# Kernel tuning notes

Hardware: AMD Instinct MI355X
Metric: run time of the kernel (lower is better)

## Reference

```python
import jax, jax.numpy as jnp
import numpy as np

N = 2048   # number of proposals
D = 128    # appearance feature dim
DK = 64    # key/query dim
DG = 64    # geometric embedding dim
SD = 8     # single relation output dim = appear_dim / N_r = 128/16


def setup_inputs() -> dict:
    key = jax.random.key(0)
    ks = jax.random.split(key, 10)
    s = jnp.float32(0.05)
    return {
        "appearance_feature": jax.random.normal(ks[0], (N, D), jnp.float32),
        "geometric_feature": jax.random.uniform(ks[1], (N, N, DG), jnp.float32),
        "Wv": jax.random.normal(ks[2], (D, SD), jnp.float32) * s,
        "bv": jnp.zeros((SD,), jnp.float32),
        "Wk": jax.random.normal(ks[3], (D, DK), jnp.float32) * s,
        "bk": jnp.zeros((DK,), jnp.float32),
        "Wq": jax.random.normal(ks[4], (D, DK), jnp.float32) * s,
        "bq": jnp.zeros((DK,), jnp.float32),
        "Wg": jax.random.normal(ks[5], (DG, 1), jnp.float32) * s,
        "bg": jnp.zeros((1,), jnp.float32),
    }


def reference(appearance_feature, geometric_feature, Wv, bv, Wk, bk, Wq, bq, Wg, bg):
    n = geometric_feature.shape[0]
    # value projection: [N, SD]
    appear = appearance_feature @ Wv + bv
    # key/query projections: [N, DK]
    k = appearance_feature @ Wk + bk
    q = appearance_feature @ Wq + bq
    # appearance attention logits: [N, N]
    w_A = (k @ q.T) * (1.0 / jnp.sqrt(jnp.float32(DK)))
    # geometric gate: relu(W_G(geom)) -> [N, N]
    w_G = jax.nn.relu(
        (geometric_feature.reshape(-1, DG) @ Wg + bg).reshape(n, n)
    )
    # gated exp, normalized over axis 0 (as in the source: torch.sum(w_nominator, 0))
    w_nom = w_G * jnp.exp(w_A)
    w = w_nom / jnp.sum(w_nom, axis=0, keepdims=True)
    # weighted sum of values: [N, SD]
    return w @ appear
```

## Files before the change

### kernel.cpp

```cpp
#include <hip/hip_runtime.h>

#define N 2048
#define D 128
#define DK 64
#define DG 64
#define SD 8
#define TI 8
#define TJ 256

typedef float f4v __attribute__((ext_vector_type(4)));

__global__ __launch_bounds__(128) void proj_kernel(
    const float* __restrict__ A,
    const float* __restrict__ Wv, const float* __restrict__ bv,
    const float* __restrict__ Wk, const float* __restrict__ bk,
    const float* __restrict__ Wq, const float* __restrict__ bq,
    float* __restrict__ kout, float* __restrict__ qout, float* __restrict__ vout)
{
    __shared__ float arow[D];
    const int i = blockIdx.x;
    const int t = threadIdx.x;
    arow[t] = A[(size_t)i * D + t];
    __syncthreads();
    for (int e = t; e < 2 * DK + SD; e += 128) {
        const float* W; const float* b; int od; int col;
        if (e < DK)            { W = Wk; b = bk; od = DK; col = e; }
        else if (e < 2 * DK)   { W = Wq; b = bq; od = DK; col = e - DK; }
        else                   { W = Wv; b = bv; od = SD; col = e - 2 * DK; }
        float acc = 0.f;
        #pragma unroll 8
        for (int c = 0; c < D; ++c) acc += arow[c] * W[c * od + col];
        acc += b[col];
        if (e < DK)          kout[(size_t)i * DK + col] = acc;
        else if (e < 2 * DK) qout[(size_t)i * DK + col] = acc;
        else                 vout[(size_t)i * SD + col] = acc;
    }
}

__global__ __launch_bounds__(256) void gate_kernel(
    const float* __restrict__ geom,
    const float* __restrict__ Wg, const float* __restrict__ bg,
    const float* __restrict__ kin, const float* __restrict__ qin,
    float* __restrict__ w_nom, float* __restrict__ colpartial)
{
    __shared__ float wA[TI * TJ];
    __shared__ float kt[TI * DK];
    const int tid = threadIdx.x;
    const int j0 = blockIdx.x * TJ;
    const int i0 = blockIdx.y * TI;

    for (int e = tid; e < TI * DK; e += 256) kt[e] = kin[(size_t)i0 * DK + e];
    __syncthreads();

    {
        float acc[TI];
        #pragma unroll
        for (int r = 0; r < TI; ++r) acc[r] = 0.f;
        const f4v* ktv = (const f4v*)kt;
        const f4v* qrow = (const f4v*)(qin + (size_t)(j0 + tid) * DK);
        f4v qv[16];
        #pragma unroll
        for (int m = 0; m < 16; ++m) qv[m] = qrow[m];
        #pragma unroll
        for (int r = 0; r < TI; ++r) {
            float p = 0.f;
            #pragma unroll
            for (int m = 0; m < 16; ++m) {
                f4v kv = ktv[r * 16 + m];
                p += kv.x * qv[m].x + kv.y * qv[m].y + kv.z * qv[m].z + kv.w * qv[m].w;
            }
            acc[r] = p;
        }
        #pragma unroll
        for (int r = 0; r < TI; ++r) wA[r * TJ + tid] = expf(acc[r] * 0.125f);
    }
    __syncthreads();

    const int group = tid >> 4;
    const int sub = tid & 15;
    const f4v wg4 = ((const f4v*)Wg)[sub];
    const float bgv = bg[0];

    float colacc[16];
    #pragma unroll
    for (int cc = 0; cc < 16; ++cc) colacc[cc] = 0.f;

    for (int ii = 0; ii < TI; ++ii) {
        const f4v* grow = (const f4v*)(geom + ((size_t)(i0 + ii) * N + j0) * DG);
        f4v g[16];
        #pragma unroll
        for (int cc = 0; cc < 16; ++cc)
            g[cc] = __builtin_nontemporal_load(grow + (size_t)(cc * 16 + group) * 16 + sub);
        #pragma unroll
        for (int cc = 0; cc < 16; ++cc) {
            float s = g[cc].x * wg4.x + g[cc].y * wg4.y + g[cc].z * wg4.z + g[cc].w * wg4.w;
            s += __shfl_xor(s, 1);
            s += __shfl_xor(s, 2);
            s += __shfl_xor(s, 4);
            s += __shfl_xor(s, 8);
            s += bgv;
            s = fmaxf(s, 0.f);
            const int jl = cc * 16 + group;
            const float val = s * wA[ii * TJ + jl];
            colacc[cc] += val;
            if (sub == 0) wA[ii * TJ + jl] = val;
        }
    }
    if (sub == 0) {
        #pragma unroll
        for (int cc = 0; cc < 16; ++cc)
            colpartial[(size_t)blockIdx.y * N + j0 + cc * 16 + group] = colacc[cc];
    }
    __syncthreads();
    {
        const f4v* src = (const f4v*)wA;
        #pragma unroll
        for (int r = 0; r < TI * TJ / 4; r += 256) {
            const int idx = r + tid;
            const int row = idx >> 6;
            const int col = idx & 63;
            ((f4v*)(w_nom + (size_t)(i0 + row) * N + j0))[col] = src[idx];
        }
    }
}

__global__ __launch_bounds__(256) void colsum_kernel(
    const float* __restrict__ colpartial, float* __restrict__ colrcp)
{
    const int j = blockIdx.x * 256 + threadIdx.x;
    float acc = 0.f;
    #pragma unroll 8
    for (int r = 0; r < N / TI; ++r) acc += colpartial[(size_t)r * N + j];
    colrcp[j] = 1.0f / acc;
}

__global__ __launch_bounds__(256) void out_kernel(
    const float* __restrict__ w_nom, const float* __restrict__ colrcp,
    const float* __restrict__ appear, float* __restrict__ out)
{
    const int i = blockIdx.x;
    const int t = threadIdx.x;
    float acc[SD];
    #pragma unroll
    for (int s = 0; s < SD; ++s) acc[s] = 0.f;

    #pragma unroll
    for (int jj = 0; jj < N / (256 * 4); ++jj) {
        const int j4 = jj * 256 + t;
        const f4v wn = ((const f4v*)(w_nom + (size_t)i * N))[j4];
        const f4v rc = ((const f4v*)colrcp)[j4];
        const float w0 = wn.x * rc.x, w1 = wn.y * rc.y, w2 = wn.z * rc.z, w3 = wn.w * rc.w;
        const int j = j4 * 4;
        const f4v* a0 = (const f4v*)(appear + (size_t)j * SD);
        f4v r0 = a0[0], r1 = a0[1];
        f4v r2 = a0[2], r3 = a0[3];
        f4v r4 = a0[4], r5 = a0[5];
        f4v r6 = a0[6], r7 = a0[7];
        acc[0] += w0 * r0.x + w1 * r2.x + w2 * r4.x + w3 * r6.x;
        acc[1] += w0 * r0.y + w1 * r2.y + w2 * r4.y + w3 * r6.y;
        acc[2] += w0 * r0.z + w1 * r2.z + w2 * r4.z + w3 * r6.z;
        acc[3] += w0 * r0.w + w1 * r2.w + w2 * r4.w + w3 * r6.w;
        acc[4] += w0 * r1.x + w1 * r3.x + w2 * r5.x + w3 * r7.x;
        acc[5] += w0 * r1.y + w1 * r3.y + w2 * r5.y + w3 * r7.y;
        acc[6] += w0 * r1.z + w1 * r3.z + w2 * r5.z + w3 * r7.z;
        acc[7] += w0 * r1.w + w1 * r3.w + w2 * r5.w + w3 * r7.w;
    }
    #pragma unroll
    for (int s = 0; s < SD; ++s) {
        #pragma unroll
        for (int off = 32; off >= 1; off >>= 1)
            acc[s] += __shfl_down(acc[s], off);
    }
    __shared__ float red[4][SD];
    const int wave = t >> 6;
    const int lane = t & 63;
    if (lane == 0) {
        #pragma unroll
        for (int s = 0; s < SD; ++s) red[wave][s] = acc[s];
    }
    __syncthreads();
    if (t < SD) out[(size_t)i * SD + t] = red[0][t] + red[1][t] + red[2][t] + red[3][t];
}

extern "C" void kernel_launch(void* const* d_in, const int* in_sizes, int n_in,
                              void* d_out, int out_size, void* d_ws, size_t ws_size,
                              hipStream_t stream) {
    const float* A    = (const float*)d_in[0];
    const float* geom = (const float*)d_in[1];
    const float* Wv   = (const float*)d_in[2];
    const float* bv   = (const float*)d_in[3];
    const float* Wk   = (const float*)d_in[4];
    const float* bk   = (const float*)d_in[5];
    const float* Wq   = (const float*)d_in[6];
    const float* bq   = (const float*)d_in[7];
    const float* Wg   = (const float*)d_in[8];
    const float* bg   = (const float*)d_in[9];
    float* out = (float*)d_out;

    float* ws = (float*)d_ws;
    float* kbuf       = ws;
    float* qbuf       = kbuf + (size_t)N * DK;
    float* appear     = qbuf + (size_t)N * DK;
    float* w_nom      = appear + (size_t)N * SD;
    float* colpartial = w_nom + (size_t)N * N;
    float* colrcp     = colpartial + (size_t)(N / TI) * N;

    proj_kernel<<<N, 128, 0, stream>>>(A, Wv, bv, Wk, bk, Wq, bq, kbuf, qbuf, appear);
    gate_kernel<<<dim3(N / TJ, N / TI), 256, 0, stream>>>(geom, Wg, bg, kbuf, qbuf,
                                                          w_nom, colpartial);
    colsum_kernel<<<N / 256, 256, 0, stream>>>(colpartial, colrcp);
    out_kernel<<<N, 256, 0, stream>>>(w_nom, colrcp, appear, out);
}
```

Baseline: 243.7 us.

## Double-buffer geometric loads and prefetch before QK compute in gate kernel

```diff
diff --git a/kernel.cpp b/kernel.cpp
--- a/kernel.cpp
+++ b/kernel.cpp
@@ -49,18 +49,52 @@
     const int j0 = blockIdx.x * TJ;
     const int i0 = blockIdx.y * TI;
 
+    const int wv  = tid >> 6;
+    const int grp = (tid >> 4) & 3;
+    const int sub = tid & 15;
+
+    const f4v* qrow = (const f4v*)(qin + (size_t)(j0 + tid) * DK);
+    f4v qv[16];
+    #pragma unroll
+    for (int m = 0; m < 16; ++m) qv[m] = qrow[m];
+
+    f4v gb0[8], gb1[8];
+
+#define G_ISSUE(buf, step) do {                                                   \
+        const int ii_ = (step) >> 1, h_ = (step) & 1;                             \
+        const f4v* grow_ = (const f4v*)(geom + ((size_t)(i0 + ii_) * N + j0) * DG);\
+        _Pragma("unroll")                                                         \
+        for (int c_ = 0; c_ < 8; ++c_) {                                          \
+            const int jl_ = wv * 64 + (h_ * 8 + c_) * 4 + grp;                    \
+            buf[c_] = grow_[(size_t)jl_ * 16 + sub];                              \
+        } } while (0)
+
+#define G_CONSUME(buf, step) do {                                                 \
+        const int ii_ = (step) >> 1, h_ = (step) & 1;                             \
+        _Pragma("unroll")                                                         \
+        for (int c_ = 0; c_ < 8; ++c_) {                                          \
+            const int cc_ = h_ * 8 + c_;                                          \
+            const int jl_ = wv * 64 + cc_ * 4 + grp;                              \
+            float s_ = buf[c_].x * wg4.x + buf[c_].y * wg4.y +                    \
+                       buf[c_].z * wg4.z + buf[c_].w * wg4.w;                     \
+            s_ += __shfl_xor(s_, 1);                                              \
+            s_ += __shfl_xor(s_, 2);                                              \
+            s_ += __shfl_xor(s_, 4);                                              \
+            s_ += __shfl_xor(s_, 8);                                              \
+            s_ = fmaxf(s_ + bgv, 0.f);                                            \
+            const float val_ = s_ * wA[ii_ * TJ + jl_];                           \
+            colacc[cc_] += val_;                                                  \
+            if (sub == 0) wA[ii_ * TJ + jl_] = val_;                              \
+        } } while (0)
+
+    G_ISSUE(gb0, 0);
+
     for (int e = tid; e < TI * DK; e += 256) kt[e] = kin[(size_t)i0 * DK + e];
     __syncthreads();
 
     {
+        const f4v* ktv = (const f4v*)kt;
         float acc[TI];
-        #pragma unroll
-        for (int r = 0; r < TI; ++r) acc[r] = 0.f;
-        const f4v* ktv = (const f4v*)kt;
-        const f4v* qrow = (const f4v*)(qin + (size_t)(j0 + tid) * DK);
-        f4v qv[16];
-        #pragma unroll
-        for (int m = 0; m < 16; ++m) qv[m] = qrow[m];
         #pragma unroll
         for (int r = 0; r < TI; ++r) {
             float p = 0.f;
@@ -76,8 +110,6 @@
     }
     __syncthreads();
 
-    const int group = tid >> 4;
-    const int sub = tid & 15;
     const f4v wg4 = ((const f4v*)Wg)[sub];
     const float bgv = bg[0];
 
@@ -85,33 +117,26 @@
     #pragma unroll
     for (int cc = 0; cc < 16; ++cc) colacc[cc] = 0.f;
 
-    for (int ii = 0; ii < TI; ++ii) {
-        const f4v* grow = (const f4v*)(geom + ((size_t)(i0 + ii) * N + j0) * DG);
-        f4v g[16];
+    #pragma unroll
+    for (int step = 0; step < 2 * TI; ++step) {
+        if ((step & 1) == 0) {
+            if (step + 1 < 2 * TI) G_ISSUE(gb1, step + 1);
+            G_CONSUME(gb0, step);
+        } else {
+            if (step + 1 < 2 * TI) G_ISSUE(gb0, step + 1);
+            G_CONSUME(gb1, step);
+        }
+    }
+#undef G_ISSUE
+#undef G_CONSUME
+
+    if (sub == 0) {
         #pragma unroll
         for (int cc = 0; cc < 16; ++cc)
-            g[cc] = __builtin_nontemporal_load(grow + (size_t)(cc * 16 + group) * 16 + sub);
-        #pragma unroll
-        for (int cc = 0; cc < 16; ++cc) {
-            float s = g[cc].x * wg4.x + g[cc].y * wg4.y + g[cc].z * wg4.z + g[cc].w * wg4.w;
-            s += __shfl_xor(s, 1);
-            s += __shfl_xor(s, 2);
-            s += __shfl_xor(s, 4);
-            s += __shfl_xor(s, 8);
-            s += bgv;
-            s = fmaxf(s, 0.f);
-            const int jl = cc * 16 + group;
-            const float val = s * wA[ii * TJ + jl];
-            colacc[cc] += val;
-            if (sub == 0) wA[ii * TJ + jl] = val;
-        }
-    }
-    if (sub == 0) {
-        #pragma unroll
-        for (int cc = 0; cc < 16; ++cc)
-            colpartial[(size_t)blockIdx.y * N + j0 + cc * 16 + group] = colacc[cc];
-    }
-    __syncthreads();
+            colpartial[(size_t)blockIdx.y * N + j0 + wv * 64 + cc * 4 + grp] = colacc[cc];
+    }
+    __syncthreads();
+
     {
         const f4v* src = (const f4v*)wA;
         #pragma unroll
```

Result: slower. 277.5 us (+13.9%).

## Stage geometric rows through swizzled double-buffered LDS with register prefetch in gate kernel

Applied to the files above, without the earlier changes.

```diff
diff --git a/kernel.cpp b/kernel.cpp
--- a/kernel.cpp
+++ b/kernel.cpp
@@ -5,8 +5,8 @@
 #define DK 64
 #define DG 64
 #define SD 8
-#define TI 8
-#define TJ 256
+#define TI 16
+#define TJ 128
 
 typedef float f4v __attribute__((ext_vector_type(4)));
 
@@ -37,27 +37,66 @@
     }
 }
 
-__global__ __launch_bounds__(256) void gate_kernel(
+__global__ __launch_bounds__(128) void gate_kernel(
     const float* __restrict__ geom,
     const float* __restrict__ Wg, const float* __restrict__ bg,
     const float* __restrict__ kin, const float* __restrict__ qin,
     float* __restrict__ w_nom, float* __restrict__ colpartial)
 {
-    __shared__ float wA[TI * TJ];
-    __shared__ float kt[TI * DK];
-    const int tid = threadIdx.x;
-    const int j0 = blockIdx.x * TJ;
-    const int i0 = blockIdx.y * TI;
-
-    for (int e = tid; e < TI * DK; e += 256) kt[e] = kin[(size_t)i0 * DK + e];
-    __syncthreads();
-
+    __shared__ float rbuf[2][TJ * DG];
+    const int tid  = threadIdx.x;
+    const int j0   = blockIdx.x * TJ;
+    const int i0   = blockIdx.y * TI;
+    const int wv   = tid >> 6;
+    const int lane = tid & 63;
+
+    const int jl_st = wv * 64 + (lane >> 4);
+    const int m_st  = lane & 15;
+    const int jl_c  = tid;
+
+    const float bgv = bg[0];
+
+    f4v s0[16], s1[16];
+
+#define G_ISSUE(S, row) do {                                                      \
+        const float* rb_ = geom + ((size_t)(i0 + (row)) * N + j0) * DG;           \
+        _Pragma("unroll")                                                         \
+        for (int t_ = 0; t_ < 16; ++t_)                                           \
+            S[t_] = *(const f4v*)(rb_ + (size_t)(jl_st + t_ * 4) * DG + m_st * 4);\
+    } while (0)
+
+#define G_WRITE(S, bufsel) do {                                                   \
+        float* b_ = &rbuf[bufsel][0];                                             \
+        _Pragma("unroll")                                                         \
+        for (int t_ = 0; t_ < 16; ++t_) {                                         \
+            const int jj_ = jl_st + t_ * 4;                                       \
+            const int pp_ = m_st ^ (jj_ & 7);                                     \
+            *(f4v*)(b_ + jj_ * DG + pp_ * 4) = S[t_];                             \
+        }                                                                         \
+    } while (0)
+
+#define G_CONSUME(bufsel, row) do {                                               \
+        const float* b_ = &rbuf[bufsel][0];                                       \
+        float sd_ = 0.f;                                                          \
+        _Pragma("unroll")                                                         \
+        for (int m_ = 0; m_ < 16; ++m_) {                                         \
+            const int pp_ = m_ ^ (jl_c & 7);                                      \
+            f4v c_ = *(const f4v*)(b_ + jl_c * DG + pp_ * 4);                     \
+            sd_ += c_.x * Wg[4 * m_]     + c_.y * Wg[4 * m_ + 1]                  \
+                 + c_.z * Wg[4 * m_ + 2] + c_.w * Wg[4 * m_ + 3];                 \
+        }                                                                         \
+        sd_ = fmaxf(sd_ + bgv, 0.f);                                              \
+        const float val_ = sd_ * expw[row];                                       \
+        colacc += val_;                                                           \
+        w_nom[(size_t)(i0 + (row)) * N + j0 + jl_c] = val_;                       \
+    } while (0)
+
+    G_ISSUE(s0, 0);
+
+    float expw[TI];
     {
-        float acc[TI];
-        #pragma unroll
-        for (int r = 0; r < TI; ++r) acc[r] = 0.f;
-        const f4v* ktv = (const f4v*)kt;
         const f4v* qrow = (const f4v*)(qin + (size_t)(j0 + tid) * DK);
+        const f4v* krow = (const f4v*)(kin + (size_t)i0 * DK);
         f4v qv[16];
         #pragma unroll
         for (int m = 0; m < 16; ++m) qv[m] = qrow[m];
@@ -66,62 +105,32 @@
             float p = 0.f;
             #pragma unroll
             for (int m = 0; m < 16; ++m) {
-                f4v kv = ktv[r * 16 + m];
-                p += kv.x * qv[m].x + kv.y * qv[m].y + kv.z * qv[m].z + kv.w * qv[m].w;
+                const f4v kf = krow[r * 16 + m];
+                p += kf.x * qv[m].x + kf.y * qv[m].y + kf.z * qv[m].z + kf.w * qv[m].w;
             }
-            acc[r] = p;
+            expw[r] = expf(p * 0.125f);
         }
-        #pragma unroll
-        for (int r = 0; r < TI; ++r) wA[r * TJ + tid] = expf(acc[r] * 0.125f);
-    }
-    __syncthreads();
-
-    const int group = tid >> 4;
-    const int sub = tid & 15;
-    const f4v wg4 = ((const f4v*)Wg)[sub];
-    const float bgv = bg[0];
-
-    float colacc[16];
-    #pragma unroll
-    for (int cc = 0; cc < 16; ++cc) colacc[cc] = 0.f;
-
-    for (int ii = 0; ii < TI; ++ii) {
-        const f4v* grow = (const f4v*)(geom + ((size_t)(i0 + ii) * N + j0) * DG);
-        f4v g[16];
-        #pragma unroll
-        for (int cc = 0; cc < 16; ++cc)
-            g[cc] = __builtin_nontemporal_load(grow + (size_t)(cc * 16 + group) * 16 + sub);
-        #pragma unroll
-        for (int cc = 0; cc < 16; ++cc) {
-            float s = g[cc].x * wg4.x + g[cc].y * wg4.y + g[cc].z * wg4.z + g[cc].w * wg4.w;
-            s += __shfl_xor(s, 1);
-            s += __shfl_xor(s, 2);
-            s += __shfl_xor(s, 4);
-            s += __shfl_xor(s, 8);
-            s += bgv;
-            s = fmaxf(s, 0.f);
-            const int jl = cc * 16 + group;
-            const float val = s * wA[ii * TJ + jl];
-            colacc[cc] += val;
-            if (sub == 0) wA[ii * TJ + jl] = val;
-        }
-    }
-    if (sub == 0) {
-        #pragma unroll
-        for (int cc = 0; cc < 16; ++cc)
-            colpartial[(size_t)blockIdx.y * N + j0 + cc * 16 + group] = colacc[cc];
-    }
-    __syncthreads();
-    {
-        const f4v* src = (const f4v*)wA;
-        #pragma unroll
-        for (int r = 0; r < TI * TJ / 4; r += 256) {
-            const int idx = r + tid;
-            const int row = idx >> 6;
-            const int col = idx & 63;
-            ((f4v*)(w_nom + (size_t)(i0 + row) * N + j0))[col] = src[idx];
-        }
-    }
+    }
+
+    float colacc = 0.f;
+    G_WRITE(s0, 0);
+    G_ISSUE(s0, 1);
+    G_ISSUE(s1, 2);
+
+    #pragma unroll
+    for (int ii = 0; ii < TI; ii += 2) {
+        G_CONSUME(0, ii);
+        G_WRITE(s0, 1);
+        if (ii + 3 < TI) G_ISSUE(s0, ii + 3);
+        G_CONSUME(1, ii + 1);
+        if (ii + 2 < TI) G_WRITE(s1, 0);
+        if (ii + 4 < TI) G_ISSUE(s1, ii + 4);
+    }
+#undef G_ISSUE
+#undef G_WRITE
+#undef G_CONSUME
+
+    colpartial[(size_t)blockIdx.y * N + j0 + tid] = colacc;
 }
 
 __global__ __launch_bounds__(256) void colsum_kernel(
@@ -206,7 +215,7 @@
     float* colrcp     = colpartial + (size_t)(N / TI) * N;
 
     proj_kernel<<<N, 128, 0, stream>>>(A, Wv, bv, Wk, bk, Wq, bq, kbuf, qbuf, appear);
-    gate_kernel<<<dim3(N / TJ, N / TI), 256, 0, stream>>>(geom, Wg, bg, kbuf, qbuf,
+    gate_kernel<<<dim3(N / TJ, N / TI), 128, 0, stream>>>(geom, Wg, bg, kbuf, qbuf,
                                                           w_nom, colpartial);
     colsum_kernel<<<N / 256, 256, 0, stream>>>(colpartial, colrcp);
     out_kernel<<<N, 256, 0, stream>>>(w_nom, colrcp, appear, out);
```

Result: slower. 304.6 us (+25.0%).

## Split exp(k·q) into separate kernel and simplify gate kernel geometry reduction

Applied to the files above, without the earlier changes.

```diff
diff --git a/kernel.cpp b/kernel.cpp
--- a/kernel.cpp
+++ b/kernel.cpp
@@ -5,8 +5,8 @@
 #define DK 64
 #define DG 64
 #define SD 8
-#define TI 8
-#define TJ 256
+#define TI 32
+#define TJ 64
 
 typedef float f4v __attribute__((ext_vector_type(4)));
 
@@ -37,91 +37,72 @@
     }
 }
 
+__global__ __launch_bounds__(256) void expa_kernel(
+    const float* __restrict__ kin, const float* __restrict__ qin,
+    float* __restrict__ expA)
+{
+    const int tid = threadIdx.x;
+    const int j0 = blockIdx.x * 256;
+    const int i0 = blockIdx.y * 16;
+
+    const f4v* qrow = (const f4v*)(qin + (size_t)(j0 + tid) * DK);
+    f4v qv[16];
+    #pragma unroll
+    for (int m = 0; m < 16; ++m) qv[m] = qrow[m];
+
+    const f4v* krow = (const f4v*)(kin + (size_t)i0 * DK);
+    #pragma unroll
+    for (int r = 0; r < 16; ++r) {
+        float p = 0.f;
+        #pragma unroll
+        for (int m = 0; m < 16; ++m) {
+            const f4v kf = krow[r * 16 + m];
+            p += kf.x * qv[m].x + kf.y * qv[m].y + kf.z * qv[m].z + kf.w * qv[m].w;
+        }
+        expA[(size_t)(i0 + r) * N + j0 + tid] = expf(p * 0.125f);
+    }
+}
+
 __global__ __launch_bounds__(256) void gate_kernel(
     const float* __restrict__ geom,
     const float* __restrict__ Wg, const float* __restrict__ bg,
-    const float* __restrict__ kin, const float* __restrict__ qin,
-    float* __restrict__ w_nom, float* __restrict__ colpartial)
+    float* __restrict__ wbuf,
+    float* __restrict__ colpartial)
 {
-    __shared__ float wA[TI * TJ];
-    __shared__ float kt[TI * DK];
     const int tid = threadIdx.x;
     const int j0 = blockIdx.x * TJ;
     const int i0 = blockIdx.y * TI;
-
-    for (int e = tid; e < TI * DK; e += 256) kt[e] = kin[(size_t)i0 * DK + e];
-    __syncthreads();
-
-    {
-        float acc[TI];
-        #pragma unroll
-        for (int r = 0; r < TI; ++r) acc[r] = 0.f;
-        const f4v* ktv = (const f4v*)kt;
-        const f4v* qrow = (const f4v*)(qin + (size_t)(j0 + tid) * DK);
-        f4v qv[16];
-        #pragma unroll
-        for (int m = 0; m < 16; ++m) qv[m] = qrow[m];
-        #pragma unroll
-        for (int r = 0; r < TI; ++r) {
-            float p = 0.f;
-            #pragma unroll
-            for (int m = 0; m < 16; ++m) {
-                f4v kv = ktv[r * 16 + m];
-                p += kv.x * qv[m].x + kv.y * qv[m].y + kv.z * qv[m].z + kv.w * qv[m].w;
-            }
-            acc[r] = p;
-        }
-        #pragma unroll
-        for (int r = 0; r < TI; ++r) wA[r * TJ + tid] = expf(acc[r] * 0.125f);
-    }
-    __syncthreads();
-
-    const int group = tid >> 4;
-    const int sub = tid & 15;
-    const f4v wg4 = ((const f4v*)Wg)[sub];
+    const int jl = tid >> 2;
+    const int c0 = tid & 3;
+    const int j  = j0 + jl;
     const float bgv = bg[0];
 
-    float colacc[16];
+    f4v wgq[4];
     #pragma unroll
-    for (int cc = 0; cc < 16; ++cc) colacc[cc] = 0.f;
+    for (int m = 0; m < 4; ++m) wgq[m] = ((const f4v*)Wg)[c0 + 4 * m];
 
+    float colacc = 0.f;
+
+    #pragma unroll 4
     for (int ii = 0; ii < TI; ++ii) {
-        const f4v* grow = (const f4v*)(geom + ((size_t)(i0 + ii) * N + j0) * DG);
-        f4v g[16];
-        #pragma unroll
-        for (int cc = 0; cc < 16; ++cc)
-            g[cc] = __builtin_nontemporal_load(grow + (size_t)(cc * 16 + group) * 16 + sub);
-        #pragma unroll
-        for (int cc = 0; cc < 16; ++cc) {
-            float s = g[cc].x * wg4.x + g[cc].y * wg4.y + g[cc].z * wg4.z + g[cc].w * wg4.w;
-            s += __shfl_xor(s, 1);
-            s += __shfl_xor(s, 2);
-            s += __shfl_xor(s, 4);
-            s += __shfl_xor(s, 8);
-            s += bgv;
-            s = fmaxf(s, 0.f);
-            const int jl = cc * 16 + group;
-            const float val = s * wA[ii * TJ + jl];
-            colacc[cc] += val;
-            if (sub == 0) wA[ii * TJ + jl] = val;
-        }
+        const float* rp = geom + ((size_t)(i0 + ii) * N + j) * DG + c0 * 4;
+        const f4v g0 = __builtin_nontemporal_load((const f4v*)(rp));
+        const f4v g1 = __builtin_nontemporal_load((const f4v*)(rp + 16));
+        const f4v g2 = __builtin_nontemporal_load((const f4v*)(rp + 32));
+        const f4v g3 = __builtin_nontemporal_load((const f4v*)(rp + 48));
+        float s = g0.x * wgq[0].x + g0.y * wgq[0].y + g0.z * wgq[0].z + g0.w * wgq[0].w
+                + g1.x * wgq[1].x + g1.y * wgq[1].y + g1.z * wgq[1].z + g1.w * wgq[1].w
+                + g2.x * wgq[2].x + g2.y * wgq[2].y + g2.z * wgq[2].z + g2.w * wgq[2].w
+                + g3.x * wgq[3].x + g3.y * wgq[3].y + g3.z * wgq[3].z + g3.w * wgq[3].w;
+        s += __shfl_xor(s, 1);
+        s += __shfl_xor(s, 2);
+        s = fmaxf(s + bgv, 0.f);
+        float* wp = wbuf + (size_t)(i0 + ii) * N + j;
+        const float val = s * (*wp);
+        colacc += val;
+        if (c0 == 0) *wp = val;
     }
-    if (sub == 0) {
-        #pragma unroll
-        for (int cc = 0; cc < 16; ++cc)
-            colpartial[(size_t)blockIdx.y * N + j0 + cc * 16 + group] = colacc[cc];
-    }
-    __syncthreads();
-    {
-        const f4v* src = (const f4v*)wA;
-        #pragma unroll
-        for (int r = 0; r < TI * TJ / 4; r += 256) {
-            const int idx = r + tid;
-            const int row = idx >> 6;
-            const int col = idx & 63;
-            ((f4v*)(w_nom + (size_t)(i0 + row) * N + j0))[col] = src[idx];
-        }
-    }
+    if (c0 == 0) colpartial[(size_t)blockIdx.y * N + j] = colacc;
 }
 
 __global__ __launch_bounds__(256) void colsum_kernel(
@@ -201,13 +182,13 @@
     float* kbuf       = ws;
     float* qbuf       = kbuf + (size_t)N * DK;
     float* appear     = qbuf + (size_t)N * DK;
-    float* w_nom      = appear + (size_t)N * SD;
-    float* colpartial = w_nom + (size_t)N * N;
+    float* wbuf       = appear + (size_t)N * SD;
+    float* colpartial = wbuf + (size_t)N * N;
     float* colrcp     = colpartial + (size_t)(N / TI) * N;
 
     proj_kernel<<<N, 128, 0, stream>>>(A, Wv, bv, Wk, bk, Wq, bq, kbuf, qbuf, appear);
-    gate_kernel<<<dim3(N / TJ, N / TI), 256, 0, stream>>>(geom, Wg, bg, kbuf, qbuf,
-                                                          w_nom, colpartial);
+    expa_kernel<<<dim3(N / 256, N / 16), 256, 0, stream>>>(kbuf, qbuf, wbuf);
+    gate_kernel<<<dim3(N / TJ, N / TI), 256, 0, stream>>>(geom, Wg, bg, wbuf, colpartial);
     colsum_kernel<<<N / 256, 256, 0, stream>>>(colpartial, colrcp);
-    out_kernel<<<N, 256, 0, stream>>>(w_nom, colrcp, appear, out);
+    out_kernel<<<N, 256, 0, stream>>>(wbuf, colrcp, appear, out);
 }
```

New measurement: 298.4 us. +22.4%, slower.
